# Kernel tuning notes

Hardware: AMD Instinct MI355X
Metric: run time of the kernel (lower is better)

The kernel has to match this reference:

```python
import jax, jax.numpy as jnp
import numpy as np

B, CIN, G, H, HW, WMIX = 128, 64, 8, 14, 16, 16  # batch, in-ch, groups, spatial, mixed width


def setup_inputs() -> dict:
    key = jax.random.key(0)
    k1, k2, k3 = jax.random.split(key, 3)
    x = jax.random.normal(k1, (B, CIN, G, H, H), dtype=jnp.float32)
    w_conv = jax.random.normal(k2, (G, 3, 3, 32), dtype=jnp.float32)   # weights[0]
    w_mix = jax.random.normal(k3, (CIN, WMIX), dtype=jnp.float32)       # weights[1]
    return {"x": x, "w_conv": w_conv, "w_mix": w_mix}


def _unfold3(t, axis, size):
    # torch F.unfold with kernel (3,1), padding (1,0) along `axis`: zero-pad by 1
    # and stack the 3 shifted windows as a new axis inserted at `axis`.
    pad = [(0, 0)] * t.ndim
    pad[axis] = (1, 1)
    p = jnp.pad(t, pad)
    slices = []
    for k in range(3):
        idx = [slice(None)] * t.ndim
        idx[axis] = slice(k, k + size)
        slices.append(p[tuple(idx)])
    return jnp.stack(slices, axis=axis)


def reference(x, w_conv, w_mix):
    # channel mix: (B, 64, 8, 14, 14) x (64, 16) -> (B, 8, 14, 14, 16)
    t4 = jnp.einsum('kjmnl,ji->kmnli', x, w_mix)
    # first unfold along H (axis 3): (B, 8, 14, 3, 14, 16)
    u1 = _unfold3(t4, 3, H)
    # second unfold along H (now axis 4): (B, 8, 14, 3, 3, 14, 16)
    u2 = _unfold3(u1, 4, H)
    # permute (0,1,2,5,4,3,6) -> (B, 8, 14, 14, 3, 3, 16)
    t5 = jnp.transpose(u2, (0, 1, 2, 5, 4, 3, 6))
    # conv channel mix: contract group(8) and both 3-taps -> (B, 14, 14, 16, 32)
    t6 = jnp.einsum('mlonikp,likj->monpj', t5, w_conv)
    # (B, 14, 14, 32, 16) -> (B, 14, 14, 512)
    t7 = jnp.transpose(t6, (0, 1, 2, 4, 3)).reshape(B, H, H, 512)
    t7 = jnp.roll(t7, 1, axis=1)  # shift_direction fixed to +1
    return jnp.transpose(t7, (0, 3, 1, 2))  # (B, 512, 14, 14)
```

## Files before the change

### kernel.cpp

```cpp
#include <hip/hip_runtime.h>

static constexpr int NB   = 128;
static constexpr int NCIN = 64;
static constexpr int NG   = 8;
static constexpr int NH   = 14;
static constexpr int NP   = 16;
static constexpr int NJ   = 32;
static constexpr int HH   = NH * NH;
static constexpr int LROW = 20;

__global__ __launch_bounds__(256) void mix_kernel(const float* __restrict__ x,
                                                  const float* __restrict__ wmix,
                                                  float* __restrict__ t4) {
    int gid = blockIdx.x * 256 + threadIdx.x;
    int ml  = gid % HH;
    int bg  = gid / HH;
    int b   = bg >> 3;
    int g   = bg & 7;

    float acc[NP];
#pragma unroll
    for (int p = 0; p < NP; p++) acc[p] = 0.f;

    const float* xb = x + (size_t)b * (NCIN * NG * HH) + (size_t)g * HH + ml;

#pragma unroll 4
    for (int j = 0; j < NCIN; j++) {
        float xv = xb[(size_t)j * (NG * HH)];
#pragma unroll
        for (int p = 0; p < NP; p++) acc[p] += xv * wmix[j * NP + p];
    }

    float* tb = t4 + (size_t)gid * NP;
#pragma unroll
    for (int p4 = 0; p4 < 4; p4++) {
        *reinterpret_cast<float4*>(tb + p4 * 4) =
            make_float4(acc[p4 * 4 + 0], acc[p4 * 4 + 1],
                        acc[p4 * 4 + 2], acc[p4 * 4 + 3]);
    }
}

__global__ __launch_bounds__(256) void conv_kernel(const float* __restrict__ t4,
                                                   const float* __restrict__ wconv,
                                                   float* __restrict__ out) {
    __shared__ __align__(16) float lds[4352];
    float* t4s = lds;
    float* w2s = lds + 2560;
    float* wcs = lds + 3840;

    const int tid   = threadIdx.x;
    const int b     = blockIdx.x / NH;
    const int o     = blockIdx.x % NH;
    const int o_src = (o + NH - 1) % NH;

    const float4* tsl4 = reinterpret_cast<const float4*>(
        t4 + ((size_t)b * NG * HH + (size_t)o_src * NH) * NP);
#pragma unroll
    for (int r = 0; r < 2; r++) {
        int idx = r * 256 + tid;
        if (idx < 448) {
            int g  = idx / 56;
            int rr = idx % 56;
            int l  = rr >> 2;
            int p0 = (rr & 3) * 4;
            float4 v = tsl4[(size_t)g * (HH * NP / 4) + rr];
            t4s[(g * 16 + p0 + 0) * LROW + (l + 2)] = v.x;
            t4s[(g * 16 + p0 + 1) * LROW + (l + 2)] = v.y;
            t4s[(g * 16 + p0 + 2) * LROW + (l + 2)] = v.z;
            t4s[(g * 16 + p0 + 3) * LROW + (l + 2)] = v.w;
        }
    }
#pragma unroll
    for (int r = 0; r < 3; r++) {
        int idx = r * 256 + tid;
        int gp  = idx / 6;
        int s   = idx % 6;
        int l2  = (s < 2) ? s : (14 + s);
        t4s[gp * LROW + l2] = 0.f;
    }
#pragma unroll
    for (int r = 0; r < 5; r++) {
        int idx = r * 256 + tid;
        int g   = idx / 160;
        int di  = (idx / 32) % 5;
        int j   = idx % 32;
        int ilo = di > 2 ? di - 2 : 0;
        int ihi = di < 2 ? di : 2;
        float s = 0.f;
        for (int i = ilo; i <= ihi; i++) {
            int k = di - i;
            s += wconv[((g * 3 + i) * 3 + k) * 32 + j];
        }
        w2s[idx] = s;
    }
#pragma unroll
    for (int r = 0; r < 2; r++) {
        int idx = r * 256 + tid;
        int sel = idx / 256;
        int g   = (idx / 32) % 8;
        int j   = idx % 32;
        wcs[idx] = wconv[(g * 9 + (sel ? 6 : 2)) * 32 + j];
    }
    __syncthreads();

    const int p  = tid & 15;
    const int jh = tid >> 4;
    const int jb = jh * 2;

    float acc[NH][2];
#pragma unroll
    for (int n = 0; n < NH; n++) { acc[n][0] = 0.f; acc[n][1] = 0.f; }

    for (int g = 0; g < NG; g++) {
        float row[LROW];
        const float* rp = &t4s[(g * 16 + p) * LROW];
#pragma unroll
        for (int q = 0; q < 5; q++) {
            float4 v = *reinterpret_cast<const float4*>(rp + q * 4);
            row[q * 4 + 0] = v.x; row[q * 4 + 1] = v.y;
            row[q * 4 + 2] = v.z; row[q * 4 + 3] = v.w;
        }
#pragma unroll
        for (int di = 0; di < 5; di++) {
            float2 w = *reinterpret_cast<const float2*>(&w2s[(g * 5 + di) * 32 + jb]);
#pragma unroll
            for (int n = 0; n < NH; n++) {
                float rv = row[n + di];
                acc[n][0] += rv * w.x;
                acc[n][1] += rv * w.y;
            }
        }
        float2 c0 = *reinterpret_cast<const float2*>(&wcs[g * 32 + jb]);
        float2 c1 = *reinterpret_cast<const float2*>(&wcs[256 + g * 32 + jb]);
        float r2 = row[2], r15 = row[15];
        acc[0][0]  -= r2  * c0.x; acc[0][1]  -= r2  * c0.y;
        acc[13][0] -= r15 * c1.x; acc[13][1] -= r15 * c1.y;
    }

    __syncthreads();

    float* obase = out + (size_t)b * 512 * HH + (size_t)o * NH;
#pragma unroll
    for (int h = 0; h < 2; h++) {
        if ((jh >> 3) == h) {
#pragma unroll
            for (int jj = 0; jj < 2; jj++) {
                int cl = (jb + jj) * 16 + p - h * 256;
#pragma unroll
                for (int n = 0; n < NH; n++) lds[cl * 15 + n] = acc[n][jj];
            }
        }
        __syncthreads();
        float* ob = obase + (size_t)(h * 256) * HH;
#pragma unroll
        for (int r = 0; r < 14; r++) {
            int idx = r * 256 + tid;
            int c   = idx / 14;
            int n   = idx % 14;
            ob[(size_t)c * HH + n] = lds[c * 15 + n];
        }
        __syncthreads();
    }
}

extern "C" void kernel_launch(void* const* d_in, const int* in_sizes, int n_in,
                              void* d_out, int out_size, void* d_ws, size_t ws_size,
                              hipStream_t stream) {
    const float* x     = (const float*)d_in[0];
    const float* wconv = (const float*)d_in[1];
    const float* wmix  = (const float*)d_in[2];
    float* out = (float*)d_out;
    float* t4  = (float*)d_ws;

    mix_kernel<<<784, 256, 0, stream>>>(x, wmix, t4);
    conv_kernel<<<NB * NH, 256, 0, stream>>>(t4, wconv, out);
}
```

Baseline: 138.1 us.

## Fuse channel-mix into conv kernel, computing t4 rows on the fly in LDS

Removes the separate mix kernel and its global t4 intermediate. Each conv block now loads the x slice for its source row, stages it in LDS in two halves of 32 input channels, and computes the 16-wide channel mix directly into the padded t4 tile. The output staging is also changed to a single pass over all 512 channels using a rotated LDS layout, which drops one round of barriers. In exchange, LDS use per block roughly doubles and there are more barriers during the mix phase, which may reduce occupancy.

```diff
diff --git a/kernel.cpp b/kernel.cpp
--- a/kernel.cpp
+++ b/kernel.cpp
@@ -5,78 +5,50 @@
 static constexpr int NG   = 8;
 static constexpr int NH   = 14;
 static constexpr int NP   = 16;
-static constexpr int NJ   = 32;
 static constexpr int HH   = NH * NH;
 static constexpr int LROW = 20;
 
-__global__ __launch_bounds__(256) void mix_kernel(const float* __restrict__ x,
-                                                  const float* __restrict__ wmix,
-                                                  float* __restrict__ t4) {
-    int gid = blockIdx.x * 256 + threadIdx.x;
-    int ml  = gid % HH;
-    int bg  = gid / HH;
-    int b   = bg >> 3;
-    int g   = bg & 7;
-
-    float acc[NP];
-#pragma unroll
-    for (int p = 0; p < NP; p++) acc[p] = 0.f;
-
-    const float* xb = x + (size_t)b * (NCIN * NG * HH) + (size_t)g * HH + ml;
-
-#pragma unroll 4
-    for (int j = 0; j < NCIN; j++) {
-        float xv = xb[(size_t)j * (NG * HH)];
-#pragma unroll
-        for (int p = 0; p < NP; p++) acc[p] += xv * wmix[j * NP + p];
-    }
-
-    float* tb = t4 + (size_t)gid * NP;
-#pragma unroll
-    for (int p4 = 0; p4 < 4; p4++) {
-        *reinterpret_cast<float4*>(tb + p4 * 4) =
-            make_float4(acc[p4 * 4 + 0], acc[p4 * 4 + 1],
-                        acc[p4 * 4 + 2], acc[p4 * 4 + 3]);
-    }
-}
-
-__global__ __launch_bounds__(256) void conv_kernel(const float* __restrict__ t4,
-                                                   const float* __restrict__ wconv,
-                                                   float* __restrict__ out) {
-    __shared__ __align__(16) float lds[4352];
-    float* t4s = lds;
-    float* w2s = lds + 2560;
-    float* wcs = lds + 3840;
+static constexpr int OFF_W2 = 0;
+static constexpr int OFF_WC = 1280;
+static constexpr int OFF_T4 = 1792;
+static constexpr int OFF_XS = 4352;
+static constexpr int OFF_WM = 8384;
+static constexpr int LDS_FLOATS = 9408;
+
+__global__ __launch_bounds__(256) void fused_kernel(const float* __restrict__ x,
+                                                    const float* __restrict__ wconv,
+                                                    const float* __restrict__ wmix,
+                                                    float* __restrict__ out) {
+    __shared__ __align__(16) float lds[LDS_FLOATS];
+    float*  w2s = lds + OFF_W2;
+    float*  wcs = lds + OFF_WC;
+    float*  t4s = lds + OFF_T4;
+    float4* xs4 = reinterpret_cast<float4*>(lds + OFF_XS);
+    float4* wm4 = reinterpret_cast<float4*>(lds + OFF_WM);
 
     const int tid   = threadIdx.x;
     const int b     = blockIdx.x / NH;
     const int o     = blockIdx.x % NH;
     const int o_src = (o + NH - 1) % NH;
 
-    const float4* tsl4 = reinterpret_cast<const float4*>(
-        t4 + ((size_t)b * NG * HH + (size_t)o_src * NH) * NP);
-#pragma unroll
-    for (int r = 0; r < 2; r++) {
-        int idx = r * 256 + tid;
-        if (idx < 448) {
-            int g  = idx / 56;
-            int rr = idx % 56;
-            int l  = rr >> 2;
-            int p0 = (rr & 3) * 4;
-            float4 v = tsl4[(size_t)g * (HH * NP / 4) + rr];
-            t4s[(g * 16 + p0 + 0) * LROW + (l + 2)] = v.x;
-            t4s[(g * 16 + p0 + 1) * LROW + (l + 2)] = v.y;
-            t4s[(g * 16 + p0 + 2) * LROW + (l + 2)] = v.z;
-            t4s[(g * 16 + p0 + 3) * LROW + (l + 2)] = v.w;
-        }
-    }
-#pragma unroll
-    for (int r = 0; r < 3; r++) {
-        int idx = r * 256 + tid;
-        int gp  = idx / 6;
-        int s   = idx % 6;
-        int l2  = (s < 2) ? s : (14 + s);
-        t4s[gp * LROW + l2] = 0.f;
+    const float* xb = x + (size_t)b * (NCIN * NG * HH) + o_src * NH;
+
+    float xr[14];
+#pragma unroll
+    for (int r = 0; r < 14; r++) {
+        int idx = r * 256 + tid;
+        int j   = idx / 112;
+        int gl  = idx % 112;
+        xr[r] = xb[(size_t)j * (NG * HH) + (gl / 14) * HH + (gl % 14)];
+    }
+
+#pragma unroll
+    for (int r = 0; r < 4; r++) {
+        int idx = r * 256 + tid;
+        int jw  = idx >> 6;
+        int p   = (idx >> 2) & 15;
+        int jj  = idx & 3;
+        lds[OFF_WM + idx] = wmix[(jw * 4 + jj) * NP + p];
     }
 #pragma unroll
     for (int r = 0; r < 5; r++) {
@@ -101,6 +73,84 @@
         int j   = idx % 32;
         wcs[idx] = wconv[(g * 9 + (sel ? 6 : 2)) * 32 + j];
     }
+#pragma unroll
+    for (int r = 0; r < 3; r++) {
+        int idx = r * 256 + tid;
+        int gp  = idx / 6;
+        int s   = idx % 6;
+        int l2  = (s < 2) ? s : (14 + s);
+        t4s[gp * LROW + l2] = 0.f;
+    }
+#pragma unroll
+    for (int r = 0; r < 14; r++) {
+        int idx  = r * 256 + tid;
+        int j    = idx / 112;
+        int gl   = idx % 112;
+        int glst = gl + (gl >> 3);
+        lds[OFF_XS + (((j >> 2) * 126 + glst) << 2) + (j & 3)] = xr[r];
+    }
+    __syncthreads();
+
+#pragma unroll
+    for (int r = 0; r < 14; r++) {
+        int idx = r * 256 + tid;
+        int j   = 32 + idx / 112;
+        int gl  = idx % 112;
+        xr[r] = xb[(size_t)j * (NG * HH) + (gl / 14) * HH + (gl % 14)];
+    }
+
+    const int  glp   = tid >> 2;
+    const int  pq    = tid & 3;
+    const bool bact  = (glp < 56);
+    const int  glst0 = glp + (glp >> 3);
+    const int  glst1 = glst0 + 63;
+    float accA[4] = {0.f, 0.f, 0.f, 0.f};
+    float accB[4] = {0.f, 0.f, 0.f, 0.f};
+
+    if (bact) {
+#pragma unroll
+        for (int j4 = 0; j4 < 8; j4++) {
+            float4 xa = xs4[j4 * 126 + glst0];
+            float4 xv = xs4[j4 * 126 + glst1];
+#pragma unroll
+            for (int pp = 0; pp < 4; pp++) {
+                float4 w = wm4[j4 * 16 + pq * 4 + pp];
+                accA[pp] += xa.x * w.x + xa.y * w.y + xa.z * w.z + xa.w * w.w;
+                accB[pp] += xv.x * w.x + xv.y * w.y + xv.z * w.z + xv.w * w.w;
+            }
+        }
+    }
+    __syncthreads();
+#pragma unroll
+    for (int r = 0; r < 14; r++) {
+        int idx  = r * 256 + tid;
+        int j    = idx / 112;
+        int gl   = idx % 112;
+        int glst = gl + (gl >> 3);
+        lds[OFF_XS + (((j >> 2) * 126 + glst) << 2) + (j & 3)] = xr[r];
+    }
+    __syncthreads();
+
+    if (bact) {
+#pragma unroll
+        for (int j4 = 0; j4 < 8; j4++) {
+            float4 xa = xs4[j4 * 126 + glst0];
+            float4 xv = xs4[j4 * 126 + glst1];
+#pragma unroll
+            for (int pp = 0; pp < 4; pp++) {
+                float4 w = wm4[(8 + j4) * 16 + pq * 4 + pp];
+                accA[pp] += xa.x * w.x + xa.y * w.y + xa.z * w.z + xa.w * w.w;
+                accB[pp] += xv.x * w.x + xv.y * w.y + xv.z * w.z + xv.w * w.w;
+            }
+        }
+        int g0 = glp / 14,        l0 = glp % 14;
+        int g1 = (glp + 56) / 14, l1 = (glp + 56) % 14;
+#pragma unroll
+        for (int pp = 0; pp < 4; pp++) {
+            t4s[(g0 * 16 + pq * 4 + pp) * LROW + l0 + 2] = accA[pp];
+            t4s[(g1 * 16 + pq * 4 + pp) * LROW + l1 + 2] = accB[pp];
+        }
+    }
     __syncthreads();
 
     const int p  = tid & 15;
@@ -139,27 +189,31 @@
 
     __syncthreads();
 
-    float* obase = out + (size_t)b * 512 * HH + (size_t)o * NH;
-#pragma unroll
-    for (int h = 0; h < 2; h++) {
-        if ((jh >> 3) == h) {
-#pragma unroll
-            for (int jj = 0; jj < 2; jj++) {
-                int cl = (jb + jj) * 16 + p - h * 256;
-#pragma unroll
-                for (int n = 0; n < NH; n++) lds[cl * 15 + n] = acc[n][jj];
-            }
-        }
-        __syncthreads();
-        float* ob = obase + (size_t)(h * 256) * HH;
-#pragma unroll
-        for (int r = 0; r < 14; r++) {
-            int idx = r * 256 + tid;
-            int c   = idx / 14;
-            int n   = idx % 14;
-            ob[(size_t)c * HH + n] = lds[c * 15 + n];
-        }
-        __syncthreads();
+#pragma unroll
+    for (int jj = 0; jj < 2; jj++) {
+        int cl  = (jb + jj) * 16 + p;
+        int rot = (cl >> 5) * 2;
+        int sb  = cl * 15;
+#pragma unroll
+        for (int n = 0; n < NH; n++) {
+            int rn = n + rot;
+            rn -= (rn >= 15) ? 15 : 0;
+            rn -= (rn >= 15) ? 15 : 0;
+            lds[sb + rn] = acc[n][jj];
+        }
+    }
+    __syncthreads();
+
+    float* ob = out + (size_t)b * 512 * HH + (size_t)o * NH;
+#pragma unroll
+    for (int r = 0; r < 28; r++) {
+        int idx = r * 256 + tid;
+        int c   = idx / 14;
+        int n   = idx % 14;
+        int rn  = n + (c >> 5) * 2;
+        rn -= (rn >= 15) ? 15 : 0;
+        rn -= (rn >= 15) ? 15 : 0;
+        ob[(size_t)c * HH + n] = lds[c * 15 + rn];
     }
 }
 
@@ -170,8 +224,7 @@
     const float* wconv = (const float*)d_in[1];
     const float* wmix  = (const float*)d_in[2];
     float* out = (float*)d_out;
-    float* t4  = (float*)d_ws;
-
-    mix_kernel<<<784, 256, 0, stream>>>(x, wmix, t4);
-    conv_kernel<<<NB * NH, 256, 0, stream>>>(t4, wconv, out);
+    (void)d_ws; (void)ws_size;
+
+    fused_kernel<<<NB * NH, 256, 0, stream>>>(x, wconv, wmix, out);
 }
```

New measurement: 147.2 us. +6.6%, slower.
